# Optimization experiments

Measured on AMD Instinct MI355X. Metric: run time of the kernel, lower is better.

## Reference

```python
import jax, jax.numpy as jnp
from jax import lax
import numpy as np

B, T = 4096, 32
VOCAB, E, H, NCLS = 10000, 300, 300, 2


def setup_inputs() -> dict:
    key = jax.random.key(0)
    ks = jax.random.split(key, 10)
    cap = jax.random.randint(ks[0], (B, T), 0, VOCAB)
    cap_len = jax.random.randint(ks[1], (B,), 1, T + 1)  # lengths in [1, T]
    embed_w = jax.random.uniform(ks[2], (VOCAB, E), jnp.float32, -0.1, 0.1)
    s = 1.0 / np.sqrt(H)
    W_ih = jax.random.uniform(ks[3], (4 * H, E), jnp.float32, -s, s)
    W_hh = jax.random.uniform(ks[4], (4 * H, H), jnp.float32, -s, s)
    b_ih = jax.random.uniform(ks[5], (4 * H,), jnp.float32, -s, s)
    b_hh = jax.random.uniform(ks[6], (4 * H,), jnp.float32, -s, s)
    cls_v = jax.random.normal(ks[7], (NCLS, H), jnp.float32) * 0.05
    cls_g = jnp.linalg.norm(cls_v, axis=1, keepdims=True)  # weight_norm init: g = ||v||
    cls_b = jax.random.uniform(ks[8], (NCLS,), jnp.float32, -s, s)
    return {"cap": cap, "cap_len": cap_len, "embed_w": embed_w,
            "W_ih": W_ih, "W_hh": W_hh, "b_ih": b_ih, "b_hh": b_hh,
            "cls_v": cls_v, "cls_g": cls_g, "cls_b": cls_b}


def _lstm_forward(cap, cap_len, embed_w, W_ih, W_hh, b_ih, b_hh, cls_v, cls_g, cls_b):
    bsz = cap.shape[0]
    hid = W_hh.shape[1]
    emb = embed_w[cap]                                   # [B, T, E]
    # Precompute the input projections for all timesteps at once (one big GEMM).
    x_gates = jnp.einsum('bte,ge->btg', emb, W_ih) + b_ih + b_hh  # [B, T, 4H]

    def step(carry, xg_t):
        h, c = carry
        gates = xg_t + h @ W_hh.T                        # [B, 4H]
        i, f, g, o = jnp.split(gates, 4, axis=-1)        # torch gate order i,f,g,o
        i = jax.nn.sigmoid(i)
        f = jax.nn.sigmoid(f)
        g = jnp.tanh(g)
        o = jax.nn.sigmoid(o)
        c = f * c + i * g
        h = o * jnp.tanh(c)
        return (h, c), h

    h0 = jnp.zeros((bsz, hid), emb.dtype)
    (_, _), hs = lax.scan(step, (h0, h0), jnp.swapaxes(x_gates, 0, 1))  # hs: [T, B, H]
    h_last = hs[cap_len - 1, jnp.arange(bsz)]            # last valid hidden state per sample
    # weight-normed classifier: W = g * v / ||v||_row  (dropout is identity in eval)
    W = cls_g * cls_v / jnp.linalg.norm(cls_v, axis=1, keepdims=True)
    return h_last @ W.T + cls_b


def reference(cap, cap_len, embed_w, W_ih, W_hh, b_ih, b_hh, cls_v, cls_g, cls_b):
    return _lstm_forward(cap, cap_len, embed_w, W_ih, W_hh, b_ih, b_hh, cls_v, cls_g, cls_b)
```

## Files before the change

kernel.cpp:

```cpp
#include <hip/hip_runtime.h>
#include <hip/hip_fp16.h>

typedef _Float16 f16;
typedef _Float16 f16x4 __attribute__((ext_vector_type(4)));
typedef _Float16 f16x8 __attribute__((ext_vector_type(8)));
typedef float f32x4 __attribute__((ext_vector_type(4)));

#define B_SZ   4096
#define T_SZ   32
#define VOCAB  10000
#define E_SZ   300
#define H_SZ   300
#define KP     320
#define GP     304
#define G4     1216
#define LDA    328
#define LDG    1224
#define LDG2   1224
#define ROWS   16
#define NBLK   (B_SZ/ROWS)

__device__ __forceinline__ float sigmoid_f(float x) {
    return 1.f / (1.f + __expf(-x));
}
__device__ __forceinline__ float tanh_f(float x) {
    x = fminf(fmaxf(x, -15.f), 15.f);
    float e = __expf(2.f * x);
    return (e - 1.f) / (e + 1.f);
}

__global__ void kP0(const float* __restrict__ ew, f16* __restrict__ embT) {
    int v = blockIdx.x, k = threadIdx.x;
    embT[(size_t)v * KP + k] = (k < E_SZ) ? (f16)ew[(size_t)v * E_SZ + k] : (f16)0.f;
}

__global__ void kPW2(const float* __restrict__ wih, const float* __restrict__ whh,
                     const float* __restrict__ bih, const float* __restrict__ bhh,
                     f16* __restrict__ Wpk, float* __restrict__ biasp) {
    int bid = blockIdx.x;
    int lane = threadIdx.x;
    int k = bid % 20, ntg = bid / 20;
    int nt = ntg % 19, gate = ntg / 19;
    int c = lane & 15, q = lane >> 4;
    int j = nt * 16 + c;
    int src = gate * H_SZ + j;
    f16 vals[8];
#pragma unroll
    for (int jj = 0; jj < 8; ++jj) {
        int kk = k * 32 + q * 8 + jj;
        float v = 0.f;
        if (j < H_SZ) {
            if (kk < KP) { if (kk < H_SZ) v = whh[(size_t)src * H_SZ + kk]; }
            else { int kx = kk - KP; if (kx < E_SZ) v = wih[(size_t)src * E_SZ + kx]; }
        }
        vals[jj] = (f16)v;
    }
    *(f16x8*)(Wpk + ((size_t)bid * 64 + lane) * 8) = *(const f16x8*)vals;
    if (k == 0 && q == 0)
        biasp[gate * GP + j] = (j < H_SZ) ? (bih[src] + bhh[src]) : 0.f;
}

__global__ void kP2(const float* __restrict__ cls_v, const float* __restrict__ cls_g,
                    float* __restrict__ Wc) {
    int lane = threadIdx.x;
    for (int cl = 0; cl < 2; ++cl) {
        float s = 0.f;
        for (int j = lane; j < H_SZ; j += 64) { float v = cls_v[cl * H_SZ + j]; s += v * v; }
        for (int off = 32; off; off >>= 1) s += __shfl_down(s, off);
        float nrm = sqrtf(__shfl(s, 0));
        float scale = cls_g[cl] / nrm;
        for (int j = lane; j < H_SZ; j += 64) Wc[cl * GP + j] = cls_v[cl * H_SZ + j] * scale;
    }
}

__global__ __launch_bounds__(512, 2)
void kX2(const f16* __restrict__ embT, const f16* __restrict__ Wpk,
         const float* __restrict__ biasp, f16* __restrict__ embX) {
    int tid = threadIdx.x;
    int v0 = blockIdx.x * 16;
    int wave = tid >> 6, lane = tid & 63;
    int c = lane & 15, q = lane >> 4;
    int gate = wave >> 1, half = wave & 1;
    int nt0 = half * 10, ntiles = half ? 9 : 10;
    const f16* wp0 = Wpk + (((size_t)(gate * 19 + nt0) * 20 + 10) * 64 + lane) * 8;
    f16x8 afr[10];
    const f16* arow = embT + (size_t)(v0 + c) * KP + q * 8;
#pragma unroll
    for (int k = 0; k < 10; ++k)
        afr[k] = *(const f16x8*)(arow + k * 32);
    f16x8 buf[10];
#pragma unroll
    for (int s = 0; s < 10; ++s)
        buf[s] = *(const f16x8*)(wp0 + (size_t)s * 512);
#pragma unroll 1
    for (int nt = 0; nt < ntiles - 1; ++nt) {
        int jcol = (nt0 + nt) * 16 + c;
        float bia = biasp[gate * GP + jcol];
        f32x4 acc = {bia, bia, bia, bia};
#pragma unroll
        for (int k = 0; k < 10; ++k) {
            acc = __builtin_amdgcn_mfma_f32_16x16x32_f16(afr[k], buf[k], acc, 0, 0, 0);
            buf[k] = *(const f16x8*)(wp0 + (size_t)(nt * 20 + k + 20) * 512);
        }
#pragma unroll
        for (int r = 0; r < 4; ++r)
            embX[((size_t)(v0 + q * 4 + r) * GP + jcol) * 4 + gate] = (f16)acc[r];
    }
    {
        int nt = ntiles - 1;
        int jcol = (nt0 + nt) * 16 + c;
        float bia = biasp[gate * GP + jcol];
        f32x4 acc = {bia, bia, bia, bia};
#pragma unroll
        for (int k = 0; k < 10; ++k)
            acc = __builtin_amdgcn_mfma_f32_16x16x32_f16(afr[k], buf[k], acc, 0, 0, 0);
#pragma unroll
        for (int r = 0; r < 4; ++r)
            embX[((size_t)(v0 + q * 4 + r) * GP + jcol) * 4 + gate] = (f16)acc[r];
    }
}

__global__ __launch_bounds__(512, 2)
void kR10(const int* __restrict__ cap,
          const int* __restrict__ cap_len,
          const f16* __restrict__ embX,
          const f16* __restrict__ Wpk,
          float* __restrict__ hlast) {
    __shared__ __align__(16) f16 hbuf[ROWS * LDA];
    __shared__ __align__(16) f16 gatesI[ROWS * LDG2];
    __shared__ int capv[ROWS * T_SZ];
    __shared__ int lens[ROWS];
    int tid = threadIdx.x;
    int b0 = blockIdx.x * ROWS;
    if (tid < ROWS) lens[tid] = cap_len[b0 + tid];
    for (int i = tid; i < ROWS * T_SZ; i += 512) capv[i] = cap[(size_t)b0 * T_SZ + i];
    for (int i = tid; i < ROWS * LDA; i += 512) hbuf[i] = (f16)0.f;
    __syncthreads();
    int wave = tid >> 6, lane = tid & 63;
    int c = lane & 15, q = lane >> 4;
    int gate = wave >> 1, half = wave & 1;
    int nt0 = half * 10, ntiles = half ? 9 : 10;
    const f16* wp0 = Wpk + ((size_t)((gate * 19 + nt0) * 20) * 64 + lane) * 8;
    const f16* hrow = hbuf + c * LDA + q * 8;
    float creg[10];
#pragma unroll
    for (int i = 0; i < 10; ++i) creg[i] = 0.f;

    for (int t = 0; t < T_SZ; ++t) {
        f16x8 afr[10];
#pragma unroll
        for (int k = 0; k < 10; ++k)
            afr[k] = *(const f16x8*)(hrow + k * 32);
        f16x8 buf[10];
#pragma unroll
        for (int s = 0; s < 10; ++s)
            buf[s] = *(const f16x8*)(wp0 + (size_t)s * 512);
#pragma unroll 1
        for (int nt = 0; nt < ntiles - 1; ++nt) {
            int jcol = (nt0 + nt) * 16 + c;
            f32x4 acc = {0.f, 0.f, 0.f, 0.f};
#pragma unroll
            for (int k = 0; k < 10; ++k) {
                acc = __builtin_amdgcn_mfma_f32_16x16x32_f16(afr[k], buf[k], acc, 0, 0, 0);
                buf[k] = *(const f16x8*)(wp0 + (size_t)(nt * 20 + k + 20) * 512);
            }
#pragma unroll
            for (int r = 0; r < 4; ++r)
                gatesI[(q * 4 + r) * LDG2 + jcol * 4 + gate] = (f16)acc[r];
        }
        {
            int nt = ntiles - 1;
            int jcol = (nt0 + nt) * 16 + c;
            f32x4 acc = {0.f, 0.f, 0.f, 0.f};
#pragma unroll
            for (int k = 0; k < 10; ++k)
                acc = __builtin_amdgcn_mfma_f32_16x16x32_f16(afr[k], buf[k], acc, 0, 0, 0);
#pragma unroll
            for (int r = 0; r < 4; ++r)
                gatesI[(q * 4 + r) * LDG2 + jcol * 4 + gate] = (f16)acc[r];
        }
        __syncthreads();
#pragma unroll
        for (int it = 0; it < 10; ++it) {
            int idx = tid + it * 512;
            int m = idx / 320, j = idx - m * 320;
            if (j < H_SZ) {
                int v = capv[m * T_SZ + t];
                f16x4 xi = *(const f16x4*)(embX + ((size_t)v * GP + j) * 4);
                f16x4 hi = *(const f16x4*)(&gatesI[m * LDG2 + j * 4]);
                float gi = (float)hi[0] + (float)xi[0];
                float gf = (float)hi[1] + (float)xi[1];
                float gg = (float)hi[2] + (float)xi[2];
                float go = (float)hi[3] + (float)xi[3];
                float ii = sigmoid_f(gi);
                float ff = sigmoid_f(gf);
                float gt = tanh_f(gg);
                float oo = sigmoid_f(go);
                float cn = ff * creg[it] + ii * gt;
                creg[it] = cn;
                float hh = oo * tanh_f(cn);
                hbuf[m * LDA + j] = (f16)hh;
                if (t == lens[m] - 1) hlast[(size_t)(b0 + m) * GP + j] = hh;
            }
        }
        __syncthreads();
    }
}

__global__ __launch_bounds__(512, 2)
void kR8(const int* __restrict__ cap,
         const int* __restrict__ cap_len,
         const f16* __restrict__ embT,
         const f16* __restrict__ Wpk,
         const float* __restrict__ biasp,
         float* __restrict__ hlast) {
    extern __shared__ __align__(16) char smem[];
    f16*   hbuf  = (f16*)smem;
    f16*   xbuf  = (f16*)(smem + 10496);
    f16*   gates = (f16*)(smem + 20992);
    float* biasL = (float*)(smem + 60160);
    int*   capv  = (int*)(smem + 65024);
    int*   lens  = (int*)(smem + 67072);
    int tid = threadIdx.x;
    int b0 = blockIdx.x * ROWS;
    if (tid < ROWS) lens[tid] = cap_len[b0 + tid];
    for (int i = tid; i < ROWS * T_SZ; i += 512) capv[i] = cap[(size_t)b0 * T_SZ + i];
    for (int i = tid; i < ROWS * LDA; i += 512) hbuf[i] = (f16)0.f;
    for (int i = tid; i < G4; i += 512) biasL[i] = biasp[i];
    __syncthreads();
    for (int i = tid; i < ROWS * 40; i += 512) {
        int m = i / 40, c8 = i - m * 40;
        int v = capv[m * T_SZ + 0];
        *(f16x8*)(xbuf + m * LDA + c8 * 8) = *(const f16x8*)(embT + (size_t)v * KP + c8 * 8);
    }
    __syncthreads();
    int wave = tid >> 6, lane = tid & 63;
    int c = lane & 15, q = lane >> 4;
    int gate = wave >> 1, half = wave & 1;
    int nt0 = half * 10, ntiles = half ? 9 : 10;
    const f16* wp0 = Wpk + ((size_t)((gate * 19 + nt0) * 20) * 64 + lane) * 8;
    const f16* hrow = hbuf + c * LDA + q * 8;
    const f16* xrow = xbuf + c * LDA + q * 8;
    float creg[10];
#pragma unroll
    for (int i = 0; i < 10; ++i) creg[i] = 0.f;

    for (int t = 0; t < T_SZ; ++t) {
        f16x8 afr[10];
#pragma unroll
        for (int k = 0; k < 10; ++k)
            afr[k] = *(const f16x8*)(hrow + k * 32);
        f16x8 buf[10];
#pragma unroll
        for (int s = 0; s < 10; ++s)
            buf[s] = *(const f16x8*)(wp0 + (size_t)s * 512);
#pragma unroll 1
        for (int nt = 0; nt < ntiles - 1; ++nt) {
            int base = nt * 20;
            int ncol = gate * GP + (nt0 + nt) * 16 + c;
            float bia = biasL[ncol];
            f32x4 acch = {bia, bia, bia, bia};
            f32x4 accx = {0.f, 0.f, 0.f, 0.f};
#pragma unroll
            for (int k = 0; k < 20; ++k) {
                if (k < 10) {
                    acch = __builtin_amdgcn_mfma_f32_16x16x32_f16(afr[k], buf[k % 10], acch, 0, 0, 0);
                } else {
                    f16x8 a = *(const f16x8*)(xrow + (k - 10) * 32);
                    accx = __builtin_amdgcn_mfma_f32_16x16x32_f16(a, buf[k % 10], accx, 0, 0, 0);
                }
                buf[k % 10] = *(const f16x8*)(wp0 + (size_t)(base + k + 10) * 512);
            }
#pragma unroll
            for (int r = 0; r < 4; ++r)
                gates[(q * 4 + r) * LDG + ncol] = (f16)(acch[r] + accx[r]);
        }
        {
            int nt = ntiles - 1;
            int base = nt * 20;
            int ncol = gate * GP + (nt0 + nt) * 16 + c;
            float bia = biasL[ncol];
            f32x4 acch = {bia, bia, bia, bia};
            f32x4 accx = {0.f, 0.f, 0.f, 0.f};
#pragma unroll
            for (int k = 0; k < 20; ++k) {
                if (k < 10) {
                    acch = __builtin_amdgcn_mfma_f32_16x16x32_f16(afr[k], buf[k % 10], acch, 0, 0, 0);
                    buf[k % 10] = *(const f16x8*)(wp0 + (size_t)(base + k + 10) * 512);
                } else {
                    f16x8 a = *(const f16x8*)(xrow + (k - 10) * 32);
                    accx = __builtin_amdgcn_mfma_f32_16x16x32_f16(a, buf[k % 10], accx, 0, 0, 0);
                }
            }
#pragma unroll
            for (int r = 0; r < 4; ++r)
                gates[(q * 4 + r) * LDG + ncol] = (f16)(acch[r] + accx[r]);
        }
        __syncthreads();
        int tp1 = t + 1;
        if (tp1 < T_SZ) {
            for (int i = tid; i < ROWS * 40; i += 512) {
                int m = i / 40, c8 = i - m * 40;
                int v = capv[m * T_SZ + tp1];
                *(f16x8*)(xbuf + m * LDA + c8 * 8) =
                    *(const f16x8*)(embT + (size_t)v * KP + c8 * 8);
            }
        }
#pragma unroll
        for (int it = 0; it < 10; ++it) {
            int idx = tid + it * 512;
            int m = idx / 320, j = idx - m * 320;
            if (j < H_SZ) {
                const f16* gr = gates + m * LDG;
                float gi = (float)gr[j];
                float gf = (float)gr[GP + j];
                float gg = (float)gr[2 * GP + j];
                float go = (float)gr[3 * GP + j];
                float ii = sigmoid_f(gi);
                float ff = sigmoid_f(gf);
                float gt = tanh_f(gg);
                float oo = sigmoid_f(go);
                float cn = ff * creg[it] + ii * gt;
                creg[it] = cn;
                float hh = oo * tanh_f(cn);
                hbuf[m * LDA + j] = (f16)hh;
                if (t == lens[m] - 1) hlast[(size_t)(b0 + m) * GP + j] = hh;
            }
        }
        __syncthreads();
    }
}

__global__ void kC(const float* __restrict__ hlast, const float* __restrict__ Wc,
                   const float* __restrict__ cls_b, float* __restrict__ out) {
    int row = blockIdx.x, lane = threadIdx.x;
    const float* h = hlast + (size_t)row * GP;
    float s0 = 0.f, s1 = 0.f;
    for (int j = lane; j < H_SZ; j += 64) {
        float hv = h[j];
        s0 += hv * Wc[j];
        s1 += hv * Wc[GP + j];
    }
    for (int off = 32; off; off >>= 1) {
        s0 += __shfl_down(s0, off);
        s1 += __shfl_down(s1, off);
    }
    if (lane == 0) {
        out[row * 2 + 0] = s0 + cls_b[0];
        out[row * 2 + 1] = s1 + cls_b[1];
    }
}

extern "C" void kernel_launch(void* const* d_in, const int* in_sizes, int n_in,
                              void* d_out, int out_size, void* d_ws, size_t ws_size,
                              hipStream_t stream) {
    const int*   cap     = (const int*)d_in[0];
    const int*   cap_len = (const int*)d_in[1];
    const float* embed_w = (const float*)d_in[2];
    const float* W_ih    = (const float*)d_in[3];
    const float* W_hh    = (const float*)d_in[4];
    const float* b_ih    = (const float*)d_in[5];
    const float* b_hh    = (const float*)d_in[6];
    const float* cls_v   = (const float*)d_in[7];
    const float* cls_g   = (const float*)d_in[8];
    const float* cls_b   = (const float*)d_in[9];
    float* out = (float*)d_out;

    char* w = (char*)d_ws;
    size_t off = 0;
    auto alloc = [&](size_t bytes) -> void* {
        void* p = w + off;
        off += (bytes + 255) & ~(size_t)255;
        return p;
    };
    f16*   embT  = (f16*)alloc((size_t)VOCAB * KP * sizeof(f16));
    f16*   Wpk   = (f16*)alloc((size_t)1520 * 64 * 8 * sizeof(f16));
    float* biasp = (float*)alloc((size_t)G4 * sizeof(float));
    float* Wc    = (float*)alloc((size_t)2 * GP * sizeof(float));
    float* hlast = (float*)alloc((size_t)B_SZ * GP * sizeof(float));
    f16*   embX  = (f16*)(w + off);
    size_t need_split = off + ((size_t)VOCAB * GP * 4 * sizeof(f16) + 255);
    bool split = (ws_size >= need_split);

    kP0<<<VOCAB, KP, 0, stream>>>(embed_w, embT);
    kPW2<<<1520, 64, 0, stream>>>(W_ih, W_hh, b_ih, b_hh, Wpk, biasp);
    kP2<<<1, 64, 0, stream>>>(cls_v, cls_g, Wc);
    if (split) {
        kX2<<<VOCAB / 16, 512, 0, stream>>>(embT, Wpk, biasp, embX);
        kR10<<<NBLK, 512, 0, stream>>>(cap, cap_len, embX, Wpk, hlast);
    } else {
        static const int smem_bytes = 67072 + 64;
        (void)hipFuncSetAttribute((const void*)kR8,
                                  hipFuncAttributeMaxDynamicSharedMemorySize, smem_bytes);
        kR8<<<NBLK, 512, smem_bytes, stream>>>(cap, cap_len, embT, Wpk, biasp, hlast);
    }
    kC<<<B_SZ, 64, 0, stream>>>(hlast, Wc, cls_b, out);
}
```

Baseline: 487.6 us.

## Process 32 batch rows per recurrent block to reuse W_hh fragments

```diff
diff --git a/kernel.cpp b/kernel.cpp
--- a/kernel.cpp
+++ b/kernel.cpp
@@ -17,16 +17,12 @@
 #define LDA    328
 #define LDG    1224
 #define LDG2   1224
-#define ROWS   16
-#define NBLK   (B_SZ/ROWS)
 
 __device__ __forceinline__ float sigmoid_f(float x) {
     return 1.f / (1.f + __expf(-x));
 }
 __device__ __forceinline__ float tanh_f(float x) {
-    x = fminf(fmaxf(x, -15.f), 15.f);
-    float e = __expf(2.f * x);
-    return (e - 1.f) / (e + 1.f);
+    return 2.f / (1.f + __expf(-2.f * x)) - 1.f;
 }
 
 __global__ void kP0(const float* __restrict__ ew, f16* __restrict__ embT) {
@@ -34,9 +30,10 @@
     embT[(size_t)v * KP + k] = (k < E_SZ) ? (f16)ew[(size_t)v * E_SZ + k] : (f16)0.f;
 }
 
-__global__ void kPW2(const float* __restrict__ wih, const float* __restrict__ whh,
+__global__ void kPW3(const float* __restrict__ wih, const float* __restrict__ whh,
                      const float* __restrict__ bih, const float* __restrict__ bhh,
-                     f16* __restrict__ Wpk, float* __restrict__ biasp) {
+                     f16* __restrict__ Wpk, f16* __restrict__ WhhS,
+                     float* __restrict__ biasp) {
     int bid = blockIdx.x;
     int lane = threadIdx.x;
     int k = bid % 20, ntg = bid / 20;
@@ -56,6 +53,8 @@
         vals[jj] = (f16)v;
     }
     *(f16x8*)(Wpk + ((size_t)bid * 64 + lane) * 8) = *(const f16x8*)vals;
+    if (k < 10)
+        *(f16x8*)(WhhS + (((size_t)ntg * 10 + k) * 64 + lane) * 8) = *(const f16x8*)vals;
     if (k == 0 && q == 0)
         biasp[gate * GP + j] = (j < H_SZ) ? (bih[src] + bhh[src]) : 0.f;
 }
@@ -121,67 +120,64 @@
 }
 
 __global__ __launch_bounds__(512, 2)
-void kR10(const int* __restrict__ cap,
+void kR11(const int* __restrict__ cap,
           const int* __restrict__ cap_len,
           const f16* __restrict__ embX,
-          const f16* __restrict__ Wpk,
+          const f16* __restrict__ WhhS,
           float* __restrict__ hlast) {
-    __shared__ __align__(16) f16 hbuf[ROWS * LDA];
-    __shared__ __align__(16) f16 gatesI[ROWS * LDG2];
-    __shared__ int capv[ROWS * T_SZ];
-    __shared__ int lens[ROWS];
+    extern __shared__ __align__(16) char smem[];
+    f16*   hbuf   = (f16*)smem;
+    f16*   gatesI = (f16*)(smem + 20992);
+    float* cbuf   = (float*)(smem + 20992 + 78336);
+    int*   capv   = (int*)(smem + 20992 + 78336 + 40960);
+    int*   lens   = (int*)(smem + 20992 + 78336 + 40960 + 4096);
     int tid = threadIdx.x;
-    int b0 = blockIdx.x * ROWS;
-    if (tid < ROWS) lens[tid] = cap_len[b0 + tid];
-    for (int i = tid; i < ROWS * T_SZ; i += 512) capv[i] = cap[(size_t)b0 * T_SZ + i];
-    for (int i = tid; i < ROWS * LDA; i += 512) hbuf[i] = (f16)0.f;
+    int b0 = blockIdx.x * 32;
+    if (tid < 32) lens[tid] = cap_len[b0 + tid];
+    for (int i = tid; i < 32 * T_SZ; i += 512) capv[i] = cap[(size_t)b0 * T_SZ + i];
+    for (int i = tid; i < 32 * LDA; i += 512) hbuf[i] = (f16)0.f;
+    for (int i = tid; i < 32 * 320; i += 512) cbuf[i] = 0.f;
     __syncthreads();
     int wave = tid >> 6, lane = tid & 63;
     int c = lane & 15, q = lane >> 4;
     int gate = wave >> 1, half = wave & 1;
     int nt0 = half * 10, ntiles = half ? 9 : 10;
-    const f16* wp0 = Wpk + ((size_t)((gate * 19 + nt0) * 20) * 64 + lane) * 8;
-    const f16* hrow = hbuf + c * LDA + q * 8;
-    float creg[10];
-#pragma unroll
-    for (int i = 0; i < 10; ++i) creg[i] = 0.f;
+    const f16* wp0 = WhhS + ((size_t)((gate * 19 + nt0) * 10) * 64 + lane) * 8;
+    const f16* hrow0 = hbuf + c * LDA + q * 8;
+    const f16* hrow1 = hbuf + (16 + c) * LDA + q * 8;
 
     for (int t = 0; t < T_SZ; ++t) {
-        f16x8 afr[10];
-#pragma unroll
-        for (int k = 0; k < 10; ++k)
-            afr[k] = *(const f16x8*)(hrow + k * 32);
         f16x8 buf[10];
 #pragma unroll
         for (int s = 0; s < 10; ++s)
             buf[s] = *(const f16x8*)(wp0 + (size_t)s * 512);
+        f16x8 afr0[10];
+#pragma unroll
+        for (int k = 0; k < 10; ++k)
+            afr0[k] = *(const f16x8*)(hrow0 + k * 32);
 #pragma unroll 1
-        for (int nt = 0; nt < ntiles - 1; ++nt) {
+        for (int nt = 0; nt < ntiles; ++nt) {
             int jcol = (nt0 + nt) * 16 + c;
-            f32x4 acc = {0.f, 0.f, 0.f, 0.f};
+            f32x4 acc0 = {0.f, 0.f, 0.f, 0.f};
+            f32x4 acc1 = {0.f, 0.f, 0.f, 0.f};
+            bool more = (nt + 1 < ntiles);
 #pragma unroll
             for (int k = 0; k < 10; ++k) {
-                acc = __builtin_amdgcn_mfma_f32_16x16x32_f16(afr[k], buf[k], acc, 0, 0, 0);
-                buf[k] = *(const f16x8*)(wp0 + (size_t)(nt * 20 + k + 20) * 512);
-            }
-#pragma unroll
-            for (int r = 0; r < 4; ++r)
-                gatesI[(q * 4 + r) * LDG2 + jcol * 4 + gate] = (f16)acc[r];
-        }
-        {
-            int nt = ntiles - 1;
-            int jcol = (nt0 + nt) * 16 + c;
-            f32x4 acc = {0.f, 0.f, 0.f, 0.f};
-#pragma unroll
-            for (int k = 0; k < 10; ++k)
-                acc = __builtin_amdgcn_mfma_f32_16x16x32_f16(afr[k], buf[k], acc, 0, 0, 0);
-#pragma unroll
-            for (int r = 0; r < 4; ++r)
-                gatesI[(q * 4 + r) * LDG2 + jcol * 4 + gate] = (f16)acc[r];
+                f16x8 a1 = *(const f16x8*)(hrow1 + k * 32);
+                acc0 = __builtin_amdgcn_mfma_f32_16x16x32_f16(afr0[k], buf[k], acc0, 0, 0, 0);
+                acc1 = __builtin_amdgcn_mfma_f32_16x16x32_f16(a1,      buf[k], acc1, 0, 0, 0);
+                if (more)
+                    buf[k] = *(const f16x8*)(wp0 + (size_t)(nt * 10 + k + 10) * 512);
+            }
+#pragma unroll
+            for (int r = 0; r < 4; ++r) {
+                gatesI[(q * 4 + r) * LDG2 + jcol * 4 + gate]        = (f16)acc0[r];
+                gatesI[(16 + q * 4 + r) * LDG2 + jcol * 4 + gate]   = (f16)acc1[r];
+            }
         }
         __syncthreads();
 #pragma unroll
-        for (int it = 0; it < 10; ++it) {
+        for (int it = 0; it < 20; ++it) {
             int idx = tid + it * 512;
             int m = idx / 320, j = idx - m * 320;
             if (j < H_SZ) {
@@ -196,8 +192,8 @@
                 float ff = sigmoid_f(gf);
                 float gt = tanh_f(gg);
                 float oo = sigmoid_f(go);
-                float cn = ff * creg[it] + ii * gt;
-                creg[it] = cn;
+                float cn = ff * cbuf[idx] + ii * gt;
+                cbuf[idx] = cn;
                 float hh = oo * tanh_f(cn);
                 hbuf[m * LDA + j] = (f16)hh;
                 if (t == lens[m] - 1) hlast[(size_t)(b0 + m) * GP + j] = hh;
@@ -222,13 +218,13 @@
     int*   capv  = (int*)(smem + 65024);
     int*   lens  = (int*)(smem + 67072);
     int tid = threadIdx.x;
-    int b0 = blockIdx.x * ROWS;
-    if (tid < ROWS) lens[tid] = cap_len[b0 + tid];
-    for (int i = tid; i < ROWS * T_SZ; i += 512) capv[i] = cap[(size_t)b0 * T_SZ + i];
-    for (int i = tid; i < ROWS * LDA; i += 512) hbuf[i] = (f16)0.f;
+    int b0 = blockIdx.x * 16;
+    if (tid < 16) lens[tid] = cap_len[b0 + tid];
+    for (int i = tid; i < 16 * T_SZ; i += 512) capv[i] = cap[(size_t)b0 * T_SZ + i];
+    for (int i = tid; i < 16 * LDA; i += 512) hbuf[i] = (f16)0.f;
     for (int i = tid; i < G4; i += 512) biasL[i] = biasp[i];
     __syncthreads();
-    for (int i = tid; i < ROWS * 40; i += 512) {
+    for (int i = tid; i < 16 * 40; i += 512) {
         int m = i / 40, c8 = i - m * 40;
         int v = capv[m * T_SZ + 0];
         *(f16x8*)(xbuf + m * LDA + c8 * 8) = *(const f16x8*)(embT + (size_t)v * KP + c8 * 8);
@@ -299,7 +295,7 @@
         __syncthreads();
         int tp1 = t + 1;
         if (tp1 < T_SZ) {
-            for (int i = tid; i < ROWS * 40; i += 512) {
+            for (int i = tid; i < 16 * 40; i += 512) {
                 int m = i / 40, c8 = i - m * 40;
                 int v = capv[m * T_SZ + tp1];
                 *(f16x8*)(xbuf + m * LDA + c8 * 8) =
@@ -375,6 +371,7 @@
     };
     f16*   embT  = (f16*)alloc((size_t)VOCAB * KP * sizeof(f16));
     f16*   Wpk   = (f16*)alloc((size_t)1520 * 64 * 8 * sizeof(f16));
+    f16*   WhhS  = (f16*)alloc((size_t)760 * 64 * 8 * sizeof(f16));
     float* biasp = (float*)alloc((size_t)G4 * sizeof(float));
     float* Wc    = (float*)alloc((size_t)2 * GP * sizeof(float));
     float* hlast = (float*)alloc((size_t)B_SZ * GP * sizeof(float));
@@ -383,16 +380,19 @@
     bool split = (ws_size >= need_split);
 
     kP0<<<VOCAB, KP, 0, stream>>>(embed_w, embT);
-    kPW2<<<1520, 64, 0, stream>>>(W_ih, W_hh, b_ih, b_hh, Wpk, biasp);
+    kPW3<<<1520, 64, 0, stream>>>(W_ih, W_hh, b_ih, b_hh, Wpk, WhhS, biasp);
     kP2<<<1, 64, 0, stream>>>(cls_v, cls_g, Wc);
     if (split) {
+        static const int smem_r11 = 20992 + 78336 + 40960 + 4096 + 128;
+        (void)hipFuncSetAttribute((const void*)kR11,
+                                  hipFuncAttributeMaxDynamicSharedMemorySize, smem_r11);
         kX2<<<VOCAB / 16, 512, 0, stream>>>(embT, Wpk, biasp, embX);
-        kR10<<<NBLK, 512, 0, stream>>>(cap, cap_len, embX, Wpk, hlast);
+        kR11<<<B_SZ / 32, 512, smem_r11, stream>>>(cap, cap_len, embX, WhhS, hlast);
     } else {
-        static const int smem_bytes = 67072 + 64;
+        static const int smem_r8 = 67072 + 64;
         (void)hipFuncSetAttribute((const void*)kR8,
-                                  hipFuncAttributeMaxDynamicSharedMemorySize, smem_bytes);
-        kR8<<<NBLK, 512, smem_bytes, stream>>>(cap, cap_len, embT, Wpk, biasp, hlast);
+                                  hipFuncAttributeMaxDynamicSharedMemorySize, smem_r8);
+        kR8<<<B_SZ / 16, 512, smem_r8, stream>>>(cap, cap_len, embT, Wpk, biasp, hlast);
     }
     kC<<<B_SZ, 64, 0, stream>>>(hlast, Wc, cls_b, out);
 }
```

Result: slower. 834.1 us (+71.1%).

## Fuse LSTM cell update into recurrent GEMM epilogue with gate-interleaved weights

Applied to the files above, without the earlier changes.

```diff
diff --git a/kernel.cpp b/kernel.cpp
--- a/kernel.cpp
+++ b/kernel.cpp
@@ -16,7 +16,7 @@
 #define G4     1216
 #define LDA    328
 #define LDG    1224
-#define LDG2   1224
+#define LDC    308
 #define ROWS   16
 #define NBLK   (B_SZ/ROWS)
 
@@ -24,9 +24,7 @@
     return 1.f / (1.f + __expf(-x));
 }
 __device__ __forceinline__ float tanh_f(float x) {
-    x = fminf(fmaxf(x, -15.f), 15.f);
-    float e = __expf(2.f * x);
-    return (e - 1.f) / (e + 1.f);
+    return 2.f / (1.f + __expf(-2.f * x)) - 1.f;
 }
 
 __global__ void kP0(const float* __restrict__ ew, f16* __restrict__ embT) {
@@ -58,6 +56,28 @@
     *(f16x8*)(Wpk + ((size_t)bid * 64 + lane) * 8) = *(const f16x8*)vals;
     if (k == 0 && q == 0)
         biasp[gate * GP + j] = (j < H_SZ) ? (bih[src] + bhh[src]) : 0.f;
+}
+
+__global__ void kPW4(const float* __restrict__ whh, f16* __restrict__ WgS) {
+    int bid = blockIdx.x;
+    int lane = threadIdx.x;
+    int c = lane & 15, q = lane >> 4;
+    f16 vals[8];
+    if (bid < 760) {
+        int nt = bid / 40, g = (bid % 40) / 10, k = bid % 10;
+        int j = nt * 16 + c;
+        int src = g * H_SZ + j;
+#pragma unroll
+        for (int jj = 0; jj < 8; ++jj) {
+            int kk = k * 32 + q * 8 + jj;
+            float v = (j < H_SZ && kk < H_SZ) ? whh[(size_t)src * H_SZ + kk] : 0.f;
+            vals[jj] = (f16)v;
+        }
+    } else {
+#pragma unroll
+        for (int jj = 0; jj < 8; ++jj) vals[jj] = (f16)0.f;
+    }
+    *(f16x8*)(WgS + ((size_t)bid * 64 + lane) * 8) = *(const f16x8*)vals;
 }
 
 __global__ void kP2(const float* __restrict__ cls_v, const float* __restrict__ cls_g,
@@ -121,89 +141,96 @@
 }
 
 __global__ __launch_bounds__(512, 2)
-void kR10(const int* __restrict__ cap,
+void kR12(const int* __restrict__ cap,
           const int* __restrict__ cap_len,
           const f16* __restrict__ embX,
-          const f16* __restrict__ Wpk,
+          const f16* __restrict__ WgS,
           float* __restrict__ hlast) {
-    __shared__ __align__(16) f16 hbuf[ROWS * LDA];
-    __shared__ __align__(16) f16 gatesI[ROWS * LDG2];
+    __shared__ __align__(16) f16 hbuf[2][ROWS * LDA];
+    __shared__ float cbuf[ROWS * LDC];
     __shared__ int capv[ROWS * T_SZ];
     __shared__ int lens[ROWS];
     int tid = threadIdx.x;
     int b0 = blockIdx.x * ROWS;
     if (tid < ROWS) lens[tid] = cap_len[b0 + tid];
     for (int i = tid; i < ROWS * T_SZ; i += 512) capv[i] = cap[(size_t)b0 * T_SZ + i];
-    for (int i = tid; i < ROWS * LDA; i += 512) hbuf[i] = (f16)0.f;
+    for (int i = tid; i < 2 * ROWS * LDA; i += 512) ((f16*)hbuf)[i] = (f16)0.f;
+    for (int i = tid; i < ROWS * LDC; i += 512) cbuf[i] = 0.f;
     __syncthreads();
     int wave = tid >> 6, lane = tid & 63;
     int c = lane & 15, q = lane >> 4;
-    int gate = wave >> 1, half = wave & 1;
-    int nt0 = half * 10, ntiles = half ? 9 : 10;
-    const f16* wp0 = Wpk + ((size_t)((gate * 19 + nt0) * 20) * 64 + lane) * 8;
-    const f16* hrow = hbuf + c * LDA + q * 8;
-    float creg[10];
-#pragma unroll
-    for (int i = 0; i < 10; ++i) creg[i] = 0.f;
+    int tstart = (wave < 5) ? 2 * wave : 10 + 3 * (wave - 5);
+    int tcnt   = (wave < 5) ? 2 : 3;
+    const f16* wp0 = WgS + ((size_t)(tstart * 40) * 64 + lane) * 8;
+    int tstop[4];
+#pragma unroll
+    for (int r = 0; r < 4; ++r) tstop[r] = lens[q * 4 + r] - 1;
+    int cur = 0;
 
     for (int t = 0; t < T_SZ; ++t) {
+        const f16* hb = hbuf[cur];
+        f16*       hn = hbuf[cur ^ 1];
         f16x8 afr[10];
 #pragma unroll
         for (int k = 0; k < 10; ++k)
-            afr[k] = *(const f16x8*)(hrow + k * 32);
+            afr[k] = *(const f16x8*)(hb + c * LDA + k * 32 + q * 8);
+        int vrow[4];
+#pragma unroll
+        for (int r = 0; r < 4; ++r) vrow[r] = capv[(q * 4 + r) * T_SZ + t];
         f16x8 buf[10];
 #pragma unroll
         for (int s = 0; s < 10; ++s)
             buf[s] = *(const f16x8*)(wp0 + (size_t)s * 512);
 #pragma unroll 1
-        for (int nt = 0; nt < ntiles - 1; ++nt) {
-            int jcol = (nt0 + nt) * 16 + c;
-            f32x4 acc = {0.f, 0.f, 0.f, 0.f};
+        for (int nt = 0; nt < tcnt; ++nt) {
+            int col = (tstart + nt) * 16 + c;
+            const f16* wnext = wp0 + (size_t)(nt * 40) * 512;
+            f32x4 acc0 = {0.f, 0.f, 0.f, 0.f};
+            f32x4 acc1 = {0.f, 0.f, 0.f, 0.f};
+            f32x4 acc2 = {0.f, 0.f, 0.f, 0.f};
+            f32x4 acc3 = {0.f, 0.f, 0.f, 0.f};
 #pragma unroll
             for (int k = 0; k < 10; ++k) {
-                acc = __builtin_amdgcn_mfma_f32_16x16x32_f16(afr[k], buf[k], acc, 0, 0, 0);
-                buf[k] = *(const f16x8*)(wp0 + (size_t)(nt * 20 + k + 20) * 512);
-            }
-#pragma unroll
-            for (int r = 0; r < 4; ++r)
-                gatesI[(q * 4 + r) * LDG2 + jcol * 4 + gate] = (f16)acc[r];
-        }
-        {
-            int nt = ntiles - 1;
-            int jcol = (nt0 + nt) * 16 + c;
-            f32x4 acc = {0.f, 0.f, 0.f, 0.f};
-#pragma unroll
-            for (int k = 0; k < 10; ++k)
-                acc = __builtin_amdgcn_mfma_f32_16x16x32_f16(afr[k], buf[k], acc, 0, 0, 0);
-#pragma unroll
-            for (int r = 0; r < 4; ++r)
-                gatesI[(q * 4 + r) * LDG2 + jcol * 4 + gate] = (f16)acc[r];
-        }
-        __syncthreads();
-#pragma unroll
-        for (int it = 0; it < 10; ++it) {
-            int idx = tid + it * 512;
-            int m = idx / 320, j = idx - m * 320;
-            if (j < H_SZ) {
-                int v = capv[m * T_SZ + t];
-                f16x4 xi = *(const f16x4*)(embX + ((size_t)v * GP + j) * 4);
-                f16x4 hi = *(const f16x4*)(&gatesI[m * LDG2 + j * 4]);
-                float gi = (float)hi[0] + (float)xi[0];
-                float gf = (float)hi[1] + (float)xi[1];
-                float gg = (float)hi[2] + (float)xi[2];
-                float go = (float)hi[3] + (float)xi[3];
+                acc0 = __builtin_amdgcn_mfma_f32_16x16x32_f16(afr[k], buf[k], acc0, 0, 0, 0);
+                buf[k] = *(const f16x8*)(wnext + (size_t)(10 + k) * 512);
+            }
+#pragma unroll
+            for (int k = 0; k < 10; ++k) {
+                acc1 = __builtin_amdgcn_mfma_f32_16x16x32_f16(afr[k], buf[k], acc1, 0, 0, 0);
+                buf[k] = *(const f16x8*)(wnext + (size_t)(20 + k) * 512);
+            }
+#pragma unroll
+            for (int k = 0; k < 10; ++k) {
+                acc2 = __builtin_amdgcn_mfma_f32_16x16x32_f16(afr[k], buf[k], acc2, 0, 0, 0);
+                buf[k] = *(const f16x8*)(wnext + (size_t)(30 + k) * 512);
+            }
+#pragma unroll
+            for (int k = 0; k < 10; ++k) {
+                acc3 = __builtin_amdgcn_mfma_f32_16x16x32_f16(afr[k], buf[k], acc3, 0, 0, 0);
+                buf[k] = *(const f16x8*)(wnext + (size_t)(40 + k) * 512);
+            }
+#pragma unroll
+            for (int r = 0; r < 4; ++r) {
+                int row = q * 4 + r;
+                f16x4 xi = *(const f16x4*)(embX + ((size_t)vrow[r] * GP + col) * 4);
+                float gi = acc0[r] + (float)xi[0];
+                float gf = acc1[r] + (float)xi[1];
+                float gg = acc2[r] + (float)xi[2];
+                float go = acc3[r] + (float)xi[3];
                 float ii = sigmoid_f(gi);
                 float ff = sigmoid_f(gf);
                 float gt = tanh_f(gg);
                 float oo = sigmoid_f(go);
-                float cn = ff * creg[it] + ii * gt;
-                creg[it] = cn;
+                int ci = row * LDC + col;
+                float cn = ff * cbuf[ci] + ii * gt;
+                cbuf[ci] = cn;
                 float hh = oo * tanh_f(cn);
-                hbuf[m * LDA + j] = (f16)hh;
-                if (t == lens[m] - 1) hlast[(size_t)(b0 + m) * GP + j] = hh;
+                hn[row * LDA + col] = (f16)hh;
+                if (t == tstop[r]) hlast[(size_t)(b0 + row) * GP + col] = hh;
             }
         }
         __syncthreads();
+        cur ^= 1;
     }
 }
 
@@ -222,13 +249,13 @@
     int*   capv  = (int*)(smem + 65024);
     int*   lens  = (int*)(smem + 67072);
     int tid = threadIdx.x;
-    int b0 = blockIdx.x * ROWS;
-    if (tid < ROWS) lens[tid] = cap_len[b0 + tid];
-    for (int i = tid; i < ROWS * T_SZ; i += 512) capv[i] = cap[(size_t)b0 * T_SZ + i];
-    for (int i = tid; i < ROWS * LDA; i += 512) hbuf[i] = (f16)0.f;
+    int b0 = blockIdx.x * 16;
+    if (tid < 16) lens[tid] = cap_len[b0 + tid];
+    for (int i = tid; i < 16 * T_SZ; i += 512) capv[i] = cap[(size_t)b0 * T_SZ + i];
+    for (int i = tid; i < 16 * LDA; i += 512) hbuf[i] = (f16)0.f;
     for (int i = tid; i < G4; i += 512) biasL[i] = biasp[i];
     __syncthreads();
-    for (int i = tid; i < ROWS * 40; i += 512) {
+    for (int i = tid; i < 16 * 40; i += 512) {
         int m = i / 40, c8 = i - m * 40;
         int v = capv[m * T_SZ + 0];
         *(f16x8*)(xbuf + m * LDA + c8 * 8) = *(const f16x8*)(embT + (size_t)v * KP + c8 * 8);
@@ -299,7 +326,7 @@
         __syncthreads();
         int tp1 = t + 1;
         if (tp1 < T_SZ) {
-            for (int i = tid; i < ROWS * 40; i += 512) {
+            for (int i = tid; i < 16 * 40; i += 512) {
                 int m = i / 40, c8 = i - m * 40;
                 int v = capv[m * T_SZ + tp1];
                 *(f16x8*)(xbuf + m * LDA + c8 * 8) =
@@ -375,6 +402,7 @@
     };
     f16*   embT  = (f16*)alloc((size_t)VOCAB * KP * sizeof(f16));
     f16*   Wpk   = (f16*)alloc((size_t)1520 * 64 * 8 * sizeof(f16));
+    f16*   WgS   = (f16*)alloc((size_t)800 * 64 * 8 * sizeof(f16));
     float* biasp = (float*)alloc((size_t)G4 * sizeof(float));
     float* Wc    = (float*)alloc((size_t)2 * GP * sizeof(float));
     float* hlast = (float*)alloc((size_t)B_SZ * GP * sizeof(float));
@@ -386,13 +414,14 @@
     kPW2<<<1520, 64, 0, stream>>>(W_ih, W_hh, b_ih, b_hh, Wpk, biasp);
     kP2<<<1, 64, 0, stream>>>(cls_v, cls_g, Wc);
     if (split) {
+        kPW4<<<800, 64, 0, stream>>>(W_hh, WgS);
         kX2<<<VOCAB / 16, 512, 0, stream>>>(embT, Wpk, biasp, embX);
-        kR10<<<NBLK, 512, 0, stream>>>(cap, cap_len, embX, Wpk, hlast);
+        kR12<<<NBLK, 512, 0, stream>>>(cap, cap_len, embX, WgS, hlast);
     } else {
-        static const int smem_bytes = 67072 + 64;
+        static const int smem_r8 = 67072 + 64;
         (void)hipFuncSetAttribute((const void*)kR8,
-                                  hipFuncAttributeMaxDynamicSharedMemorySize, smem_bytes);
-        kR8<<<NBLK, 512, smem_bytes, stream>>>(cap, cap_len, embT, Wpk, biasp, hlast);
+                                  hipFuncAttributeMaxDynamicSharedMemorySize, smem_r8);
+        kR8<<<B_SZ / 16, 512, smem_r8, stream>>>(cap, cap_len, embT, Wpk, biasp, hlast);
     }
     kC<<<B_SZ, 64, 0, stream>>>(hlast, Wc, cls_b, out);
 }
```

Measured after the change: 507.5 us. +4.1%, slower.
